# Optimization experiments

Measured on AMD Instinct MI355X. Metric: run time of the kernel, lower is better.

Reference implementation:

```python
import jax, jax.numpy as jnp
import numpy as np

EMBD = 512
HEADS = 8
HEAD = EMBD // HEADS


def setup_inputs() -> dict:
    key = jax.random.key(0)
    ks = jax.random.split(key, 9)
    B, M = 4, 2048
    s = 1.0 / np.sqrt(EMBD)
    inp = {
        "x": jax.random.normal(ks[0], (B, M, EMBD), dtype=jnp.float32),
        "wq": jax.random.uniform(ks[1], (EMBD, EMBD), jnp.float32, -s, s),
        "bq": jnp.zeros((EMBD,), jnp.float32),
        "wk": jax.random.uniform(ks[2], (EMBD, EMBD), jnp.float32, -s, s),
        "bk": jnp.zeros((EMBD,), jnp.float32),
        "wv": jax.random.uniform(ks[3], (EMBD, EMBD), jnp.float32, -s, s),
        "bv": jnp.zeros((EMBD,), jnp.float32),
        "wo": jax.random.uniform(ks[4], (EMBD, EMBD), jnp.float32, -s, s),
        "bo": jnp.zeros((EMBD,), jnp.float32),
        "gamma": jnp.ones((EMBD,), jnp.float32),
        "beta": jnp.zeros((EMBD,), jnp.float32),
    }
    return inp


def layer_norm(x, gamma, beta, eps=1e-5):
    mu = jnp.mean(x, axis=-1, keepdims=True)
    var = jnp.mean(jnp.square(x - mu), axis=-1, keepdims=True)
    return (x - mu) * jax.lax.rsqrt(var + eps) * gamma + beta


def reference(x, wq, bq, wk, bk, wv, bv, wo, bo, gamma, beta):
    B, M, _ = x.shape
    norm = layer_norm(x, gamma, beta)
    # projections; reshape to [B, H, M, Dh]
    def proj(w, b):
        return (norm @ w.T + b).reshape(B, M, HEADS, HEAD).transpose(0, 2, 1, 3)
    q = proj(wq, bq)
    k = proj(wk, bk)
    v = proj(wv, bv)
    scores = jnp.einsum("bhmd,bhnd->bhmn", q, k) / np.sqrt(HEAD)
    # exclude self-attention on the diagonal
    diag = jnp.eye(M, dtype=bool)
    scores = jnp.where(diag, -jnp.inf, scores)
    attn = jax.nn.softmax(scores, axis=-1)
    ctx = jnp.einsum("bhmn,bhnd->bhmd", attn, v)
    ctx = ctx.transpose(0, 2, 1, 3).reshape(B, M, EMBD)
    out = ctx @ wo.T + bo
    return (out + x, attn)
```

## Files before the change

### kernel.cpp

```cpp
#include <hip/hip_runtime.h>

#define B_   4
#define H_   8
#define M_   2048
#define D_   512
#define DH_  64

typedef short  bf16x8 __attribute__((ext_vector_type(8)));
typedef float  f32x4  __attribute__((ext_vector_type(4)));
typedef unsigned short u16x4 __attribute__((ext_vector_type(4)));
typedef unsigned int   u32x2 __attribute__((ext_vector_type(2)));

#define EXPC 0.18033688011112042f

static __device__ __forceinline__ unsigned short f2bf(float f) {
  unsigned u = __float_as_uint(f);
  u += 0x7fffu + ((u >> 16) & 1u);
  return (unsigned short)(u >> 16);
}

static __device__ __forceinline__ unsigned cvtpk(float lo, float hi) {
  unsigned r;
  asm("v_cvt_pk_bf16_f32 %0, %1, %2" : "=v"(r) : "v"(lo), "v"(hi));
  return r;
}

static __device__ __forceinline__ int swz128(int row, int byteoff) {
  return row * 128 + (byteoff ^ ((row & 7) << 4));
}

static __device__ __forceinline__ void glds16(const void* g, void* l) {
  __builtin_amdgcn_global_load_lds(
      (const __attribute__((address_space(1))) unsigned*)g,
      (__attribute__((address_space(3))) unsigned*)l, 16, 0, 0);
}

static __device__ __forceinline__ void stage_tile(
    const char* g0, size_t rstride, char* lds, int t) {
  const int r0 = t >> 3, c0 = t & 7;
  const char* src = g0 + (size_t)r0 * rstride + ((c0 ^ (r0 & 7)) << 4);
  char* dst = lds + ((t & 192) << 4);
  #pragma unroll
  for (int c = 0; c < 4; ++c)
    glds16(src + (size_t)c * 32 * rstride, dst + c * 4096);
}

__global__ __launch_bounds__(256) void ln_kernel(
    const float* __restrict__ x, const float* __restrict__ gamma,
    const float* __restrict__ beta, unsigned short* __restrict__ xn)
{
  int row = blockIdx.x;
  int t = threadIdx.x;
  const float* xr = x + (size_t)row * D_;
  float v0 = xr[t], v1 = xr[t + 256];
  float s = v0 + v1, ss = v0 * v0 + v1 * v1;
  #pragma unroll
  for (int m = 1; m < 64; m <<= 1) {
    s  += __shfl_xor(s, m);
    ss += __shfl_xor(ss, m);
  }
  __shared__ float red[8];
  int wid = t >> 6;
  if ((t & 63) == 0) { red[wid] = s; red[wid + 4] = ss; }
  __syncthreads();
  s  = red[0] + red[1] + red[2] + red[3];
  ss = red[4] + red[5] + red[6] + red[7];
  float mu  = s * (1.0f / D_);
  float var = ss * (1.0f / D_) - mu * mu;
  float rstd = rsqrtf(var + 1e-5f);
  unsigned short* o = xn + (size_t)row * D_;
  o[t]       = f2bf((v0 - mu) * rstd * gamma[t]       + beta[t]);
  o[t + 256] = f2bf((v1 - mu) * rstd * gamma[t + 256] + beta[t + 256]);
}

__global__ __launch_bounds__(256) void cast_w_kernel(
    const float* __restrict__ wq, const float* __restrict__ wk,
    const float* __restrict__ wv, const float* __restrict__ wo,
    unsigned short* __restrict__ wqkv, unsigned short* __restrict__ wob)
{
  int i = blockIdx.x * 256 + threadIdx.x;
  wqkv[i]          = f2bf(wq[i]);
  wqkv[i + 262144] = f2bf(wk[i]);
  wqkv[i + 524288] = f2bf(wv[i]);
  wob[i]           = f2bf(wo[i]);
}

__global__ __launch_bounds__(256) void qkv_gemm(
    const unsigned short* __restrict__ xn,
    const unsigned short* __restrict__ wqkv,
    const float* __restrict__ bq, const float* __restrict__ bk,
    const float* __restrict__ bv,
    unsigned short* __restrict__ q, unsigned short* __restrict__ k,
    unsigned short* __restrict__ vT)
{
  __shared__ __align__(16) char As[128 * 128];
  __shared__ __align__(16) char Bs[128 * 128];
  const int m0 = blockIdx.x * 128;
  const int n0 = blockIdx.y * 128;
  const int t = threadIdx.x, wid = t >> 6, lane = t & 63;
  const int wr = (wid >> 1) * 64, wc = (wid & 1) * 64;
  const int cl = lane & 15, rg = lane >> 4;
  const f32x4 z4 = {0.f, 0.f, 0.f, 0.f};
  const bool isv = (n0 >= 1024);

  const char* agb = (const char*)xn   + (size_t)m0 * 1024;
  const char* bgb = (const char*)wqkv + (size_t)n0 * 1024;

  f32x4 acc[4][4];
  #pragma unroll
  for (int i = 0; i < 4; ++i)
    #pragma unroll
    for (int j = 0; j < 4; ++j) acc[i][j] = z4;

  for (int k0 = 0; k0 < 512; k0 += 64) {
    __syncthreads();
    stage_tile(agb + k0 * 2, 1024, As, t);
    stage_tile(bgb + k0 * 2, 1024, Bs, t);
    __syncthreads();
    #pragma unroll
    for (int ks = 0; ks < 2; ++ks) {
      int koff = ks * 64 + rg * 16;
      bf16x8 af[4], bfr[4];
      #pragma unroll
      for (int i = 0; i < 4; ++i)
        af[i] = *(const bf16x8*)(As + swz128(wr + i * 16 + cl, koff));
      #pragma unroll
      for (int j = 0; j < 4; ++j)
        bfr[j] = *(const bf16x8*)(Bs + swz128(wc + j * 16 + cl, koff));
      if (isv) {
        #pragma unroll
        for (int i = 0; i < 4; ++i)
          #pragma unroll
          for (int j = 0; j < 4; ++j)
            acc[i][j] = __builtin_amdgcn_mfma_f32_16x16x32_bf16(af[i], bfr[j], acc[i][j], 0, 0, 0);
      } else {
        #pragma unroll
        for (int j = 0; j < 4; ++j)
          #pragma unroll
          for (int i = 0; i < 4; ++i)
            acc[j][i] = __builtin_amdgcn_mfma_f32_16x16x32_bf16(bfr[j], af[i], acc[j][i], 0, 0, 0);
      }
    }
  }

  if (isv) {
    #pragma unroll
    for (int j = 0; j < 4; ++j) {
      int n = n0 + wc + j * 16 + cl;
      int nn = n & 511;
      int h = nn >> 6, dh = nn & 63;
      float bias = bv[nn];
      #pragma unroll
      for (int i = 0; i < 4; ++i) {
        int mrow = m0 + wr + i * 16 + rg * 4;
        int b = mrow >> 11, mm = mrow & 2047;
        u32x2 u;
        u[0] = cvtpk(acc[i][j][0] + bias, acc[i][j][1] + bias);
        u[1] = cvtpk(acc[i][j][2] + bias, acc[i][j][3] + bias);
        *(u32x2*)(vT + ((size_t)(b * H_ + h) * DH_ + dh) * M_ + mm) = u;
      }
    }
  } else {
    const int mat = n0 >> 9;
    unsigned short* dst = mat ? k : q;
    const float* bias = mat ? bk : bq;
    #pragma unroll
    for (int j = 0; j < 4; ++j) {
      int nn0 = ((n0 + wc) & 511) + j * 16 + rg * 4;
      int h = nn0 >> 6, dh = nn0 & 63;
      f32x4 b4 = *(const f32x4*)(bias + nn0);
      #pragma unroll
      for (int i = 0; i < 4; ++i) {
        int mrow = m0 + wr + i * 16 + cl;
        int b = mrow >> 11, mm = mrow & 2047;
        u32x2 u;
        u[0] = cvtpk(acc[j][i][0] + b4[0], acc[j][i][1] + b4[1]);
        u[1] = cvtpk(acc[j][i][2] + b4[2], acc[j][i][3] + b4[3]);
        *(u32x2*)(dst + ((size_t)(b * H_ + h) * M_ + mm) * DH_ + dh) = u;
      }
    }
  }
}

__global__ __launch_bounds__(256, 8) void psum_kernel(
    const unsigned short* __restrict__ q, const unsigned short* __restrict__ k,
    float* __restrict__ rinv)
{
  __shared__ __align__(16) char Kb[2][8192];
  const int flat = blockIdx.x;
  const int bh = (flat & 7) * 4 + ((flat >> 3) >> 5);
  const int mb = (flat >> 3) & 31;
  const int m0 = mb * 64;
  const int t = threadIdx.x, wid = t >> 6, lane = t & 63;
  const int wr = wid * 16, cl = lane & 15, rg = lane >> 4;
  const char* qb = (const char*)(q + (size_t)bh * M_ * DH_);
  const char* kb = (const char*)(k + (size_t)bh * M_ * DH_);
  const int m_g = m0 + wr + cl;
  const f32x4 z4 = {0.f, 0.f, 0.f, 0.f};

  bf16x8 qf[2];
  #pragma unroll
  for (int ks = 0; ks < 2; ++ks)
    qf[ks] = *(const bf16x8*)(qb + (size_t)m_g * 128 + ks * 64 + rg * 16);

  const int r0 = t >> 3, c0 = t & 7;
  const int ldsoff = (t & 192) * 16;
  const size_t sK0 = (size_t)r0 * 128 + ((c0 ^ (r0 & 7)) << 4);

  glds16(kb + sK0,        Kb[0] + ldsoff);
  glds16(kb + sK0 + 4096, Kb[0] + ldsoff + 4096);

  float psum = 0.f;
  int buf = 0;
  for (int nt = 0; nt < 32; ++nt) {
    __syncthreads();
    if (nt + 1 < 32) {
      const char* src = kb + (size_t)(nt + 1) * 8192;
      glds16(src + sK0,        Kb[buf ^ 1] + ldsoff);
      glds16(src + sK0 + 4096, Kb[buf ^ 1] + ldsoff + 4096);
    }
    f32x4 s[4];
    #pragma unroll
    for (int j = 0; j < 4; ++j) s[j] = z4;
    #pragma unroll
    for (int ks = 0; ks < 2; ++ks)
      #pragma unroll
      for (int j = 0; j < 4; ++j) {
        bf16x8 kf = *(const bf16x8*)(Kb[buf] + swz128(j * 16 + cl, ks * 64 + rg * 16));
        s[j] = __builtin_amdgcn_mfma_f32_16x16x32_bf16(kf, qf[ks], s[j], 0, 0, 0);
      }
    if (nt == mb) {
      #pragma unroll
      for (int j = 0; j < 4; ++j)
        #pragma unroll
        for (int r = 0; r < 4; ++r) {
          int n_g = nt * 64 + j * 16 + rg * 4 + r;
          float p = __builtin_amdgcn_exp2f(s[j][r] * EXPC);
          psum += (n_g == m_g) ? 0.f : p;
        }
    } else {
      #pragma unroll
      for (int j = 0; j < 4; ++j)
        #pragma unroll
        for (int r = 0; r < 4; ++r)
          psum += __builtin_amdgcn_exp2f(s[j][r] * EXPC);
    }
    buf ^= 1;
  }
  psum += __shfl_xor(psum, 16);
  psum += __shfl_xor(psum, 32);
  if (lane < 16) rinv[bh * M_ + m_g] = 1.0f / psum;
}

__global__ __launch_bounds__(256, 4) void attn_kernel(
    const unsigned short* __restrict__ q,
    const unsigned short* __restrict__ k,
    const unsigned short* __restrict__ vT,
    const float* __restrict__ rinv,
    float* __restrict__ attn,
    unsigned short* __restrict__ ctx)
{
  __shared__ __align__(16) char Kb[2][8192];
  __shared__ __align__(16) char Vb[2][8192];
  __shared__ __align__(16) char Ps[4][2048];

  const int flat = blockIdx.x;
  const int bh = (flat & 7) * 4 + ((flat >> 3) >> 5);
  const int mb = (flat >> 3) & 31;
  const int m0 = mb * 64;
  const int t = threadIdx.x, wid = t >> 6, lane = t & 63;
  const int wr = wid * 16, cl = lane & 15, rg = lane >> 4;
  const int m_g = m0 + wr + cl;
  const f32x4 z4 = {0.f, 0.f, 0.f, 0.f};

  const char* qb = (const char*)(q  + (size_t)bh * M_ * DH_);
  const char* kb = (const char*)(k  + (size_t)bh * M_ * DH_);
  const char* vb = (const char*)(vT + (size_t)bh * DH_ * M_);
  float* ab = attn + (size_t)bh * M_ * M_;

  const float rv = rinv[bh * M_ + m_g];
  bf16x8 qf[2];
  #pragma unroll
  for (int ks = 0; ks < 2; ++ks)
    qf[ks] = *(const bf16x8*)(qb + (size_t)m_g * 128 + ks * 64 + rg * 16);

  const int r0 = t >> 3, c0 = t & 7;
  const int ldsoff = (t & 192) * 16;
  const size_t sK0 = (size_t)r0 * 128 + ((c0 ^ (r0 & 7)) << 4);
  const size_t sV0 = (size_t)r0 * (M_ * 2) + ((c0 ^ (r0 & 7)) << 4);

  glds16(kb + sK0,                    Kb[0] + ldsoff);
  glds16(kb + sK0 + 4096,             Kb[0] + ldsoff + 4096);
  glds16(vb + sV0,                    Vb[0] + ldsoff);
  glds16(vb + sV0 + 32 * (M_ * 2),    Vb[0] + ldsoff + 4096);
  __syncthreads();

  f32x4 oc[4];
  #pragma unroll
  for (int j = 0; j < 4; ++j) oc[j] = z4;

  const int srow = lane >> 4;
  const int sch  = lane & 15;

  int buf = 0;
  for (int nt = 0; nt < 32; ++nt) {
    if (nt + 1 < 32) {
      const char* srcK = kb + (size_t)(nt + 1) * 8192;
      const char* srcV = vb + (size_t)(nt + 1) * 128;
      glds16(srcK + sK0,                 Kb[buf ^ 1] + ldsoff);
      glds16(srcK + sK0 + 4096,          Kb[buf ^ 1] + ldsoff + 4096);
      glds16(srcV + sV0,                 Vb[buf ^ 1] + ldsoff);
      glds16(srcV + sV0 + 32 * (M_ * 2), Vb[buf ^ 1] + ldsoff + 4096);
    }
    f32x4 s[4];
    #pragma unroll
    for (int j = 0; j < 4; ++j) s[j] = z4;
    #pragma unroll
    for (int ks = 0; ks < 2; ++ks)
      #pragma unroll
      for (int j = 0; j < 4; ++j) {
        bf16x8 kf = *(const bf16x8*)(Kb[buf] + swz128(j * 16 + cl, ks * 64 + rg * 16));
        s[j] = __builtin_amdgcn_mfma_f32_16x16x32_bf16(kf, qf[ks], s[j], 0, 0, 0);
      }
    const bool dtile = (nt == mb);
    #pragma unroll
    for (int j = 0; j < 4; ++j) {
      f32x4 pv;
      #pragma unroll
      for (int r = 0; r < 4; ++r) {
        int n_g = nt * 64 + j * 16 + rg * 4 + r;
        float p = __builtin_amdgcn_exp2f(s[j][r] * EXPC) * rv;
        pv[r] = (dtile && n_g == m_g) ? 0.f : p;
      }
      u32x2 u;
      u[0] = cvtpk(pv[0], pv[1]);
      u[1] = cvtpk(pv[2], pv[3]);
      *(u32x2*)(Ps[wid] + swz128(cl, j * 32 + rg * 8)) = u;
    }
    {
      float* abase = ab + ((size_t)(m0 + wr + srow)) * M_ + nt * 64 + sch * 4;
      #pragma unroll
      for (int it = 0; it < 4; ++it) {
        u16x4 pu = *(const u16x4*)(Ps[wid] + swz128(it * 4 + srow, sch * 8));
        f32x4 pv;
        #pragma unroll
        for (int r = 0; r < 4; ++r) pv[r] = __uint_as_float((unsigned)pu[r] << 16);
        __builtin_nontemporal_store(pv, (f32x4*)(abase + (size_t)it * 4 * M_));
      }
    }
    #pragma unroll
    for (int ks = 0; ks < 2; ++ks) {
      bf16x8 pf = *(const bf16x8*)(Ps[wid] + swz128(cl, ks * 64 + rg * 16));
      #pragma unroll
      for (int jd = 0; jd < 4; ++jd) {
        bf16x8 vf = *(const bf16x8*)(Vb[buf] + swz128(jd * 16 + cl, ks * 64 + rg * 16));
        oc[jd] = __builtin_amdgcn_mfma_f32_16x16x32_bf16(vf, pf, oc[jd], 0, 0, 0);
      }
    }
    if (nt + 1 < 32) {
      asm volatile("s_waitcnt vmcnt(4) lgkmcnt(0)" ::: "memory");
      __builtin_amdgcn_s_barrier();
    }
    buf ^= 1;
  }

  int b = bh >> 3, h = bh & 7;
  unsigned short* crow = ctx + ((size_t)b * M_ + m_g) * D_ + h * DH_ + rg * 4;
  #pragma unroll
  for (int jd = 0; jd < 4; ++jd) {
    u32x2 u;
    u[0] = cvtpk(oc[jd][0], oc[jd][1]);
    u[1] = cvtpk(oc[jd][2], oc[jd][3]);
    *(u32x2*)(crow + jd * 16) = u;
  }
}

__global__ __launch_bounds__(256) void out_gemm(
    const unsigned short* __restrict__ ctxb,
    const unsigned short* __restrict__ wob,
    const float* __restrict__ bo,
    const float* __restrict__ x,
    float* __restrict__ out)
{
  __shared__ __align__(16) char As[128 * 128];
  __shared__ __align__(16) char Bs[128 * 128];
  const int m0 = blockIdx.x * 128;
  const int n0 = blockIdx.y * 128;
  const int t = threadIdx.x, wid = t >> 6, lane = t & 63;
  const int wr = (wid >> 1) * 64, wc = (wid & 1) * 64;
  const int cl = lane & 15, rg = lane >> 4;
  const f32x4 z4 = {0.f, 0.f, 0.f, 0.f};

  const char* agb = (const char*)ctxb + (size_t)m0 * 1024;
  const char* bgb = (const char*)wob  + (size_t)n0 * 1024;

  f32x4 acc[4][4];
  #pragma unroll
  for (int j = 0; j < 4; ++j)
    #pragma unroll
    for (int i = 0; i < 4; ++i) acc[j][i] = z4;

  for (int k0 = 0; k0 < 512; k0 += 64) {
    __syncthreads();
    stage_tile(agb + k0 * 2, 1024, As, t);
    stage_tile(bgb + k0 * 2, 1024, Bs, t);
    __syncthreads();
    #pragma unroll
    for (int ks = 0; ks < 2; ++ks) {
      int koff = ks * 64 + rg * 16;
      bf16x8 af[4], bfr[4];
      #pragma unroll
      for (int i = 0; i < 4; ++i)
        af[i] = *(const bf16x8*)(As + swz128(wr + i * 16 + cl, koff));
      #pragma unroll
      for (int j = 0; j < 4; ++j)
        bfr[j] = *(const bf16x8*)(Bs + swz128(wc + j * 16 + cl, koff));
      #pragma unroll
      for (int j = 0; j < 4; ++j)
        #pragma unroll
        for (int i = 0; i < 4; ++i)
          acc[j][i] = __builtin_amdgcn_mfma_f32_16x16x32_bf16(bfr[j], af[i], acc[j][i], 0, 0, 0);
    }
  }

  #pragma unroll
  for (int j = 0; j < 4; ++j) {
    int nb = n0 + wc + j * 16 + rg * 4;
    f32x4 bo4 = *(const f32x4*)(bo + nb);
    #pragma unroll
    for (int i = 0; i < 4; ++i) {
      int m = m0 + wr + i * 16 + cl;
      f32x4 x4 = *(const f32x4*)(x + (size_t)m * 512 + nb);
      f32x4 o;
      #pragma unroll
      for (int r = 0; r < 4; ++r) o[r] = acc[j][i][r] + bo4[r] + x4[r];
      *(f32x4*)(out + (size_t)m * 512 + nb) = o;
    }
  }
}

extern "C" void kernel_launch(void* const* d_in, const int* in_sizes, int n_in,
                              void* d_out, int out_size, void* d_ws, size_t ws_size,
                              hipStream_t stream) {
  const float* x     = (const float*)d_in[0];
  const float* wq    = (const float*)d_in[1];
  const float* bq    = (const float*)d_in[2];
  const float* wk    = (const float*)d_in[3];
  const float* bk    = (const float*)d_in[4];
  const float* wv    = (const float*)d_in[5];
  const float* bv    = (const float*)d_in[6];
  const float* wo    = (const float*)d_in[7];
  const float* bo    = (const float*)d_in[8];
  const float* gamma = (const float*)d_in[9];
  const float* beta  = (const float*)d_in[10];

  char* ws = (char*)d_ws;
  unsigned short* xn   = (unsigned short*)(ws);
  unsigned short* wqkv = (unsigned short*)(ws + 8388608);
  float*          rinv = (float*)(ws + 8388608);
  unsigned short* wob  = (unsigned short*)(ws + 9961472);
  unsigned short* qb   = (unsigned short*)(ws + 10485760);
  unsigned short* kb   = (unsigned short*)(ws + 18874368);
  unsigned short* vT   = (unsigned short*)(ws + 27262976);
  unsigned short* ctx  = (unsigned short*)(ws + 35651584);

  float* out  = (float*)d_out;
  float* attn = (float*)d_out + 4194304;

  ln_kernel<<<8192, 256, 0, stream>>>(x, gamma, beta, xn);
  cast_w_kernel<<<1024, 256, 0, stream>>>(wq, wk, wv, wo, wqkv, wob);
  qkv_gemm<<<dim3(64, 12), 256, 0, stream>>>(xn, wqkv, bq, bk, bv, qb, kb, vT);
  psum_kernel<<<1024, 256, 0, stream>>>(qb, kb, rinv);
  attn_kernel<<<1024, 256, 0, stream>>>(qb, kb, vT, rinv, attn, ctx);
  out_gemm<<<dim3(64, 4), 256, 0, stream>>>(ctx, wob, bo, x, out);
}
```

Baseline: 213.5 us.

## Pre-pack K/V into MFMA fragment layout and fuse row-sum pass into attention

New measurement: 201.6 us. 5.6% less time.

```diff
diff --git a/kernel.cpp b/kernel.cpp
--- a/kernel.cpp
+++ b/kernel.cpp
@@ -7,6 +7,7 @@
 #define DH_  64
 
 typedef short  bf16x8 __attribute__((ext_vector_type(8)));
+typedef short  bf16x4 __attribute__((ext_vector_type(4)));
 typedef float  f32x4  __attribute__((ext_vector_type(4)));
 typedef unsigned short u16x4 __attribute__((ext_vector_type(4)));
 typedef unsigned int   u32x2 __attribute__((ext_vector_type(2)));
@@ -23,6 +24,11 @@
   unsigned r;
   asm("v_cvt_pk_bf16_f32 %0, %1, %2" : "=v"(r) : "v"(lo), "v"(hi));
   return r;
+}
+
+static __device__ __forceinline__ f32x4 mfma16(bf16x4 a, bf16x4 b, f32x4 c) {
+  asm("v_mfma_f32_16x16x16_bf16 %0, %1, %2, %0" : "+v"(c) : "v"(a), "v"(b));
+  return c;
 }
 
 static __device__ __forceinline__ int swz128(int row, int byteoff) {
@@ -90,8 +96,8 @@
     const unsigned short* __restrict__ wqkv,
     const float* __restrict__ bq, const float* __restrict__ bk,
     const float* __restrict__ bv,
-    unsigned short* __restrict__ q, unsigned short* __restrict__ k,
-    unsigned short* __restrict__ vT)
+    unsigned short* __restrict__ q, unsigned short* __restrict__ Kp,
+    unsigned short* __restrict__ Vp)
 {
   __shared__ __align__(16) char As[128 * 128];
   __shared__ __align__(16) char Bs[128 * 128];
@@ -149,26 +155,29 @@
       int n = n0 + wc + j * 16 + cl;
       int nn = n & 511;
       int h = nn >> 6, dh = nn & 63;
+      int jd = dh >> 4, cld = dh & 15;
       float bias = bv[nn];
       #pragma unroll
       for (int i = 0; i < 4; ++i) {
         int mrow = m0 + wr + i * 16 + rg * 4;
         int b = mrow >> 11, mm = mrow & 2047;
+        int nt = mm >> 6, nl = mm & 63;
+        int jp = nl >> 5, half = (nl >> 4) & 1, rgv = (nl >> 2) & 3;
         u32x2 u;
         u[0] = cvtpk(acc[i][j][0] + bias, acc[i][j][1] + bias);
         u[1] = cvtpk(acc[i][j][2] + bias, acc[i][j][3] + bias);
-        *(u32x2*)(vT + ((size_t)(b * H_ + h) * DH_ + dh) * M_ + mm) = u;
+        size_t off = ((((size_t)(b * H_ + h) * 32 + nt) * 4 + jd) * 2 + jp) * 512
+                   + (rgv * 16 + cld) * 8 + half * 4;
+        *(u16x4*)(Vp + off) = __builtin_bit_cast(u16x4, u);
       }
     }
   } else {
     const int mat = n0 >> 9;
-    unsigned short* dst = mat ? k : q;
-    const float* bias = mat ? bk : bq;
     #pragma unroll
     for (int j = 0; j < 4; ++j) {
       int nn0 = ((n0 + wc) & 511) + j * 16 + rg * 4;
       int h = nn0 >> 6, dh = nn0 & 63;
-      f32x4 b4 = *(const f32x4*)(bias + nn0);
+      f32x4 b4 = *(const f32x4*)((mat ? bk : bq) + nn0);
       #pragma unroll
       for (int i = 0; i < 4; ++i) {
         int mrow = m0 + wr + i * 16 + cl;
@@ -176,92 +185,27 @@
         u32x2 u;
         u[0] = cvtpk(acc[j][i][0] + b4[0], acc[j][i][1] + b4[1]);
         u[1] = cvtpk(acc[j][i][2] + b4[2], acc[j][i][3] + b4[3]);
-        *(u32x2*)(dst + ((size_t)(b * H_ + h) * M_ + mm) * DH_ + dh) = u;
-      }
-    }
-  }
-}
-
-__global__ __launch_bounds__(256, 8) void psum_kernel(
-    const unsigned short* __restrict__ q, const unsigned short* __restrict__ k,
-    float* __restrict__ rinv)
-{
-  __shared__ __align__(16) char Kb[2][8192];
-  const int flat = blockIdx.x;
-  const int bh = (flat & 7) * 4 + ((flat >> 3) >> 5);
-  const int mb = (flat >> 3) & 31;
-  const int m0 = mb * 64;
-  const int t = threadIdx.x, wid = t >> 6, lane = t & 63;
-  const int wr = wid * 16, cl = lane & 15, rg = lane >> 4;
-  const char* qb = (const char*)(q + (size_t)bh * M_ * DH_);
-  const char* kb = (const char*)(k + (size_t)bh * M_ * DH_);
-  const int m_g = m0 + wr + cl;
-  const f32x4 z4 = {0.f, 0.f, 0.f, 0.f};
-
-  bf16x8 qf[2];
-  #pragma unroll
-  for (int ks = 0; ks < 2; ++ks)
-    qf[ks] = *(const bf16x8*)(qb + (size_t)m_g * 128 + ks * 64 + rg * 16);
-
-  const int r0 = t >> 3, c0 = t & 7;
-  const int ldsoff = (t & 192) * 16;
-  const size_t sK0 = (size_t)r0 * 128 + ((c0 ^ (r0 & 7)) << 4);
-
-  glds16(kb + sK0,        Kb[0] + ldsoff);
-  glds16(kb + sK0 + 4096, Kb[0] + ldsoff + 4096);
-
-  float psum = 0.f;
-  int buf = 0;
-  for (int nt = 0; nt < 32; ++nt) {
-    __syncthreads();
-    if (nt + 1 < 32) {
-      const char* src = kb + (size_t)(nt + 1) * 8192;
-      glds16(src + sK0,        Kb[buf ^ 1] + ldsoff);
-      glds16(src + sK0 + 4096, Kb[buf ^ 1] + ldsoff + 4096);
-    }
-    f32x4 s[4];
-    #pragma unroll
-    for (int j = 0; j < 4; ++j) s[j] = z4;
-    #pragma unroll
-    for (int ks = 0; ks < 2; ++ks)
-      #pragma unroll
-      for (int j = 0; j < 4; ++j) {
-        bf16x8 kf = *(const bf16x8*)(Kb[buf] + swz128(j * 16 + cl, ks * 64 + rg * 16));
-        s[j] = __builtin_amdgcn_mfma_f32_16x16x32_bf16(kf, qf[ks], s[j], 0, 0, 0);
-      }
-    if (nt == mb) {
-      #pragma unroll
-      for (int j = 0; j < 4; ++j)
-        #pragma unroll
-        for (int r = 0; r < 4; ++r) {
-          int n_g = nt * 64 + j * 16 + rg * 4 + r;
-          float p = __builtin_amdgcn_exp2f(s[j][r] * EXPC);
-          psum += (n_g == m_g) ? 0.f : p;
+        if (mat == 0) {
+          *(u16x4*)(q + ((size_t)(b * H_ + h) * M_ + mm) * DH_ + dh) =
+              __builtin_bit_cast(u16x4, u);
+        } else {
+          int ks = dh >> 5, rgk = (dh >> 3) & 3, e0 = dh & 7;
+          size_t off = ((((size_t)(b * H_ + h) * 32 + (mm >> 6)) * 4 + ((mm >> 4) & 3)) * 2 + ks) * 512
+                     + (rgk * 16 + (mm & 15)) * 8 + e0;
+          *(u16x4*)(Kp + off) = __builtin_bit_cast(u16x4, u);
         }
-    } else {
-      #pragma unroll
-      for (int j = 0; j < 4; ++j)
-        #pragma unroll
-        for (int r = 0; r < 4; ++r)
-          psum += __builtin_amdgcn_exp2f(s[j][r] * EXPC);
-    }
-    buf ^= 1;
-  }
-  psum += __shfl_xor(psum, 16);
-  psum += __shfl_xor(psum, 32);
-  if (lane < 16) rinv[bh * M_ + m_g] = 1.0f / psum;
+      }
+    }
+  }
 }
 
 __global__ __launch_bounds__(256, 4) void attn_kernel(
     const unsigned short* __restrict__ q,
-    const unsigned short* __restrict__ k,
-    const unsigned short* __restrict__ vT,
-    const float* __restrict__ rinv,
+    const unsigned short* __restrict__ Kp,
+    const unsigned short* __restrict__ Vp,
     float* __restrict__ attn,
     unsigned short* __restrict__ ctx)
 {
-  __shared__ __align__(16) char Kb[2][8192];
-  __shared__ __align__(16) char Vb[2][8192];
   __shared__ __align__(16) char Ps[4][2048];
 
   const int flat = blockIdx.x;
@@ -273,27 +217,49 @@
   const int m_g = m0 + wr + cl;
   const f32x4 z4 = {0.f, 0.f, 0.f, 0.f};
 
-  const char* qb = (const char*)(q  + (size_t)bh * M_ * DH_);
-  const char* kb = (const char*)(k  + (size_t)bh * M_ * DH_);
-  const char* vb = (const char*)(vT + (size_t)bh * DH_ * M_);
+  const char* qb = (const char*)(q + (size_t)bh * M_ * DH_);
+  const unsigned short* kpb = Kp + (size_t)bh * 131072;
+  const unsigned short* vpb = Vp + (size_t)bh * 131072;
   float* ab = attn + (size_t)bh * M_ * M_;
 
-  const float rv = rinv[bh * M_ + m_g];
   bf16x8 qf[2];
   #pragma unroll
   for (int ks = 0; ks < 2; ++ks)
     qf[ks] = *(const bf16x8*)(qb + (size_t)m_g * 128 + ks * 64 + rg * 16);
 
-  const int r0 = t >> 3, c0 = t & 7;
-  const int ldsoff = (t & 192) * 16;
-  const size_t sK0 = (size_t)r0 * 128 + ((c0 ^ (r0 & 7)) << 4);
-  const size_t sV0 = (size_t)r0 * (M_ * 2) + ((c0 ^ (r0 & 7)) << 4);
-
-  glds16(kb + sK0,                    Kb[0] + ldsoff);
-  glds16(kb + sK0 + 4096,             Kb[0] + ldsoff + 4096);
-  glds16(vb + sV0,                    Vb[0] + ldsoff);
-  glds16(vb + sV0 + 32 * (M_ * 2),    Vb[0] + ldsoff + 4096);
-  __syncthreads();
+  float psum = 0.f;
+  for (int nt = 0; nt < 32; ++nt) {
+    const unsigned short* kch = kpb + (size_t)nt * 4096;
+    f32x4 s[4];
+    #pragma unroll
+    for (int j = 0; j < 4; ++j) s[j] = z4;
+    #pragma unroll
+    for (int ks = 0; ks < 2; ++ks)
+      #pragma unroll
+      for (int j = 0; j < 4; ++j) {
+        bf16x8 kf = *(const bf16x8*)(kch + (j * 2 + ks) * 512 + lane * 8);
+        s[j] = __builtin_amdgcn_mfma_f32_16x16x32_bf16(kf, qf[ks], s[j], 0, 0, 0);
+      }
+    if (nt == mb) {
+      #pragma unroll
+      for (int j = 0; j < 4; ++j)
+        #pragma unroll
+        for (int r = 0; r < 4; ++r) {
+          int n_g = nt * 64 + j * 16 + rg * 4 + r;
+          float p = __builtin_amdgcn_exp2f(s[j][r] * EXPC);
+          psum += (n_g == m_g) ? 0.f : p;
+        }
+    } else {
+      #pragma unroll
+      for (int j = 0; j < 4; ++j)
+        #pragma unroll
+        for (int r = 0; r < 4; ++r)
+          psum += __builtin_amdgcn_exp2f(s[j][r] * EXPC);
+    }
+  }
+  psum += __shfl_xor(psum, 16);
+  psum += __shfl_xor(psum, 32);
+  const float rv = 1.0f / psum;
 
   f32x4 oc[4];
   #pragma unroll
@@ -302,16 +268,11 @@
   const int srow = lane >> 4;
   const int sch  = lane & 15;
 
-  int buf = 0;
+  asm volatile("s_nop 7" :::);
+
   for (int nt = 0; nt < 32; ++nt) {
-    if (nt + 1 < 32) {
-      const char* srcK = kb + (size_t)(nt + 1) * 8192;
-      const char* srcV = vb + (size_t)(nt + 1) * 128;
-      glds16(srcK + sK0,                 Kb[buf ^ 1] + ldsoff);
-      glds16(srcK + sK0 + 4096,          Kb[buf ^ 1] + ldsoff + 4096);
-      glds16(srcV + sV0,                 Vb[buf ^ 1] + ldsoff);
-      glds16(srcV + sV0 + 32 * (M_ * 2), Vb[buf ^ 1] + ldsoff + 4096);
-    }
+    const unsigned short* kch = kpb + (size_t)nt * 4096;
+    const unsigned short* vch = vpb + (size_t)nt * 4096;
     f32x4 s[4];
     #pragma unroll
     for (int j = 0; j < 4; ++j) s[j] = z4;
@@ -319,10 +280,11 @@
     for (int ks = 0; ks < 2; ++ks)
       #pragma unroll
       for (int j = 0; j < 4; ++j) {
-        bf16x8 kf = *(const bf16x8*)(Kb[buf] + swz128(j * 16 + cl, ks * 64 + rg * 16));
+        bf16x8 kf = *(const bf16x8*)(kch + (j * 2 + ks) * 512 + lane * 8);
         s[j] = __builtin_amdgcn_mfma_f32_16x16x32_bf16(kf, qf[ks], s[j], 0, 0, 0);
       }
     const bool dtile = (nt == mb);
+    bf16x4 pb[4];
     #pragma unroll
     for (int j = 0; j < 4; ++j) {
       f32x4 pv;
@@ -335,6 +297,7 @@
       u32x2 u;
       u[0] = cvtpk(pv[0], pv[1]);
       u[1] = cvtpk(pv[2], pv[3]);
+      pb[j] = __builtin_bit_cast(bf16x4, u);
       *(u32x2*)(Ps[wid] + swz128(cl, j * 32 + rg * 8)) = u;
     }
     {
@@ -349,20 +312,18 @@
       }
     }
     #pragma unroll
-    for (int ks = 0; ks < 2; ++ks) {
-      bf16x8 pf = *(const bf16x8*)(Ps[wid] + swz128(cl, ks * 64 + rg * 16));
+    for (int jp = 0; jp < 2; ++jp)
       #pragma unroll
       for (int jd = 0; jd < 4; ++jd) {
-        bf16x8 vf = *(const bf16x8*)(Vb[buf] + swz128(jd * 16 + cl, ks * 64 + rg * 16));
-        oc[jd] = __builtin_amdgcn_mfma_f32_16x16x32_bf16(vf, pf, oc[jd], 0, 0, 0);
-      }
-    }
-    if (nt + 1 < 32) {
-      asm volatile("s_waitcnt vmcnt(4) lgkmcnt(0)" ::: "memory");
-      __builtin_amdgcn_s_barrier();
-    }
-    buf ^= 1;
-  }
+        bf16x8 w = *(const bf16x8*)(vch + (jd * 2 + jp) * 512 + lane * 8);
+        bf16x4 vlo = __builtin_shufflevector(w, w, 0, 1, 2, 3);
+        bf16x4 vhi = __builtin_shufflevector(w, w, 4, 5, 6, 7);
+        oc[jd] = mfma16(vlo, pb[jp * 2],     oc[jd]);
+        oc[jd] = mfma16(vhi, pb[jp * 2 + 1], oc[jd]);
+      }
+  }
+
+  asm volatile("s_nop 7\n\ts_nop 7" :::);
 
   int b = bh >> 3, h = bh & 7;
   unsigned short* crow = ctx + ((size_t)b * M_ + m_g) * D_ + h * DH_ + rg * 4;
@@ -457,11 +418,10 @@
   char* ws = (char*)d_ws;
   unsigned short* xn   = (unsigned short*)(ws);
   unsigned short* wqkv = (unsigned short*)(ws + 8388608);
-  float*          rinv = (float*)(ws + 8388608);
   unsigned short* wob  = (unsigned short*)(ws + 9961472);
   unsigned short* qb   = (unsigned short*)(ws + 10485760);
-  unsigned short* kb   = (unsigned short*)(ws + 18874368);
-  unsigned short* vT   = (unsigned short*)(ws + 27262976);
+  unsigned short* Kp   = (unsigned short*)(ws + 18874368);
+  unsigned short* Vp   = (unsigned short*)(ws + 27262976);
   unsigned short* ctx  = (unsigned short*)(ws + 35651584);
 
   float* out  = (float*)d_out;
@@ -469,8 +429,7 @@
 
   ln_kernel<<<8192, 256, 0, stream>>>(x, gamma, beta, xn);
   cast_w_kernel<<<1024, 256, 0, stream>>>(wq, wk, wv, wo, wqkv, wob);
-  qkv_gemm<<<dim3(64, 12), 256, 0, stream>>>(xn, wqkv, bq, bk, bv, qb, kb, vT);
-  psum_kernel<<<1024, 256, 0, stream>>>(qb, kb, rinv);
-  attn_kernel<<<1024, 256, 0, stream>>>(qb, kb, vT, rinv, attn, ctx);
+  qkv_gemm<<<dim3(64, 12), 256, 0, stream>>>(xn, wqkv, bq, bk, bv, qb, Kp, Vp);
+  attn_kernel<<<1024, 256, 0, stream>>>(qb, Kp, Vp, attn, ctx);
   out_gemm<<<dim3(64, 4), 256, 0, stream>>>(ctx, wob, bo, x, out);
 }
```
